# Kernel tuning notes

Measured on AMD Instinct MI355X. Metric: run time of the kernel, lower is better.

## Reference

```python
import math
import jax, jax.numpy as jnp
import numpy as np

WS = [2048, 4096, 8192]
RS = [1, 2, 4]
HEAD_IDX = 0


def build_indices(n):
    """Static dilated gather indices: concat of every segment's strided slice.

    Matches _prepare_sparse_indices for the chosen (ws, rs, n), which yields
    zero padding (each segment contributes exactly max_subatt_n indices).
    """
    max_m = min(n, max(w // r for w, r in zip(WS, RS)))
    parts = []
    for w, r in zip(WS, RS):
        offset = HEAD_IDX % r
        for s in range(0, n, w):
            seg = np.arange(s, min(s + w, n))[offset::r]
            assert len(seg) == max_m, "config chosen to avoid padding"
            parts.append(seg)
    return np.concatenate(parts).astype(np.int32), max_m


def _forward(x, Wq, Wk, Wv):
    b, n, c = x.shape
    idx_np, m = build_indices(n)
    idx = jnp.asarray(idx_np)            # [S], S = num_subatt * m
    S = idx_np.shape[0]
    nb = S // m                          # number of sub-attention windows

    # gather -> [b, S, c] -> batched windows [b*nb, m, c]
    bx = x[:, idx, :].reshape(b * nb, m, c)

    # single-head causal attention on each window, also return softmax denoms
    scale = 1.0 / math.sqrt(c)
    q = bx @ Wq
    k = bx @ Wk
    v = bx @ Wv
    logits = jnp.einsum('bqc,bkc->bqk', q, k) * scale
    causal = jnp.tril(jnp.ones((m, m), dtype=bool))
    logits = jnp.where(causal, logits, -jnp.inf)
    lse = jax.scipy.special.logsumexp(logits, axis=-1)   # [b*nb, m]
    probs = jnp.exp(logits - lse[..., None])
    o = jnp.einsum('bqk,bkc->bqc', probs, v)             # [b*nb, m, c]
    denoms = jnp.exp(lse)                                 # softmax denominators

    o = o.reshape(b, S, c)
    denoms = denoms.reshape(b, S)

    # _mix_outputs: scatter-add denoms per target position, reweight, scatter-add outputs
    denom_sums = jnp.zeros((b, n), x.dtype).at[:, idx].add(denoms)
    alphas = denoms / denom_sums[:, idx]                  # [b, S]
    out = jnp.zeros((b, n, c), x.dtype).at[:, idx, :].add(o * alphas[..., None])
    return out


def setup_inputs() -> dict:
    key = jax.random.key(0)
    kx, kq, kk, kv = jax.random.split(key, 4)
    b, n, c = 4, 8192, 64
    s = 1.0 / math.sqrt(c)
    return {
        'x': jax.random.normal(kx, (b, n, c), dtype=jnp.float32),
        'Wq': jax.random.normal(kq, (c, c), dtype=jnp.float32) * s,
        'Wk': jax.random.normal(kk, (c, c), dtype=jnp.float32) * s,
        'Wv': jax.random.normal(kv, (c, c), dtype=jnp.float32) * s,
    }


def reference(x, Wq, Wk, Wv):
    return _forward(x, Wq, Wk, Wv)
```

## Files before the change

### kernel.cpp

```cpp
#include <hip/hip_runtime.h>
#include <math.h>

#define NB   4
#define NSEQ 8192
#define CDIM 64
#define M    2048
#define NW   7
#define NBLK2 40

typedef _Float16 half8 __attribute__((ext_vector_type(8)));
typedef __fp16 fp16x2 __attribute__((ext_vector_type(2)));
typedef float f32x4 __attribute__((ext_vector_type(4)));
typedef unsigned short u16x4 __attribute__((ext_vector_type(4)));

#if defined(__has_builtin) && __has_builtin(__builtin_amdgcn_exp2f)
#define EXP2(x) __builtin_amdgcn_exp2f(x)
#else
#define EXP2(x) __expf((x) * 0.69314718056f)
#endif

#define QSCALE 0.1803368801111204f
#define PBIAS 4.0f

#define K_OFF   0
#define VT_OFF  8192
#define VT_STRIDE 80
#define VT_BUF  5120

__device__ __forceinline__ int win_base(int w) {
    return (w < 4) ? (w << 11) : ((w < 6) ? ((w - 4) << 12) : 0);
}
__device__ __forceinline__ int win_stride(int w) {
    return (w < 4) ? 1 : ((w < 6) ? 2 : 4);
}

__global__ __launch_bounds__(256, 1) void qkv_proj(
        const float* __restrict__ x,
        const float* __restrict__ Wq, const float* __restrict__ Wk,
        const float* __restrict__ Wv,
        _Float16* __restrict__ Qg, _Float16* __restrict__ Kg,
        _Float16* __restrict__ Vg) {
    const int t = threadIdx.x;
    const int wid = t >> 6, lane = t & 63, l15 = lane & 15, quad = lane >> 4;

    half8 wb[3][2][4];
#pragma unroll
    for (int m = 0; m < 3; ++m) {
        const float* Wm = (m == 0) ? Wq : ((m == 1) ? Wk : Wv);
        const float sc = (m == 0) ? QSCALE : 1.0f;
#pragma unroll
        for (int kh = 0; kh < 2; ++kh)
#pragma unroll
            for (int nt = 0; nt < 4; ++nt) {
                float f[8];
#pragma unroll
                for (int j = 0; j < 8; ++j)
                    f[j] = Wm[(kh * 32 + quad * 8 + j) * 64 + nt * 16 + l15] * sc;
                union { fp16x2 h[4]; half8 v; } u;
#pragma unroll
                for (int p = 0; p < 4; ++p)
                    u.h[p] = __builtin_amdgcn_cvt_pkrtz(f[2 * p], f[2 * p + 1]);
                wb[m][kh][nt] = u.v;
            }
    }

    const int rowbase = blockIdx.x * 128 + wid * 32;
#pragma unroll
    for (int mt = 0; mt < 2; ++mt) {
        const int r0 = rowbase + mt * 16;
        half8 xa[2];
#pragma unroll
        for (int kh = 0; kh < 2; ++kh) {
            const float* xr = x + (size_t)(r0 + l15) * 64 + kh * 32 + quad * 8;
            const float4 a = *(const float4*)xr;
            const float4 b2 = *(const float4*)(xr + 4);
            union { fp16x2 h[4]; half8 v; } u;
            u.h[0] = __builtin_amdgcn_cvt_pkrtz(a.x, a.y);
            u.h[1] = __builtin_amdgcn_cvt_pkrtz(a.z, a.w);
            u.h[2] = __builtin_amdgcn_cvt_pkrtz(b2.x, b2.y);
            u.h[3] = __builtin_amdgcn_cvt_pkrtz(b2.z, b2.w);
            xa[kh] = u.v;
        }
#pragma unroll
        for (int m = 0; m < 3; ++m) {
            f32x4 acc[4];
#pragma unroll
            for (int nt = 0; nt < 4; ++nt) {
                acc[nt] = (f32x4){0.f, 0.f, 0.f, 0.f};
                acc[nt] = __builtin_amdgcn_mfma_f32_16x16x32_f16(xa[0], wb[m][0][nt], acc[nt], 0, 0, 0);
                acc[nt] = __builtin_amdgcn_mfma_f32_16x16x32_f16(xa[1], wb[m][1][nt], acc[nt], 0, 0, 0);
            }
            _Float16* outp = (m == 0) ? Qg : ((m == 1) ? Kg : Vg);
#pragma unroll
            for (int nt = 0; nt < 4; ++nt)
#pragma unroll
                for (int j = 0; j < 4; ++j)
                    outp[(size_t)(r0 + quad * 4 + j) * 64 + nt * 16 + l15] =
                        (_Float16)acc[nt][j];
        }
    }
}

__global__ __launch_bounds__(256, 4) void attn(
        const _Float16* __restrict__ Qg, const _Float16* __restrict__ Kg,
        const _Float16* __restrict__ Vg,
        _Float16* __restrict__ Op, float* __restrict__ LSEp) {
    __shared__ __align__(16) char smem[18432];

    int id = 39 - (int)blockIdx.x;
    int QT, ci;
    if (id < 4)       { QT = id;              ci = 0; }
    else if (id < 12) { int r = id - 4;  QT = 4  + (r >> 1); ci = r & 1; }
    else if (id < 24) { int r = id - 12; int q3 = r / 3; QT = 8 + q3; ci = r - 3 * q3; }
    else              { int r = id - 24; QT = 12 + (r >> 2); ci = r & 3; }
    const int w = blockIdx.y, b = blockIdx.z;
    const int base = win_base(w), stride = win_stride(w);
    const int g = QT >> 2;
    const int cb = 2 * g * (g + 1) + (QT & 3) * (g + 1);
    const int outblk = (b * NW + w) * NBLK2 + cb + ci;
    const int kt0 = ci * 16;
    const int ktmax = 4 * QT + 4;
    const int kt1 = (kt0 + 16 < ktmax) ? kt0 + 16 : ktmax;

    const _Float16* Qb = Qg + (size_t)b * NSEQ * 64;
    const _Float16* Kb = Kg + (size_t)b * NSEQ * 64;
    const _Float16* Vb = Vg + (size_t)b * NSEQ * 64;

    const int t = threadIdx.x;
    const int wid = t >> 6, lane = t & 63, l15 = lane & 15, quad = lane >> 4;

    const int sr = t >> 3, sch = t & 7;
    const int c4 = t & 15, kq = t >> 4;
    const int vd0 = 4 * c4;

    const size_t qr0 = (size_t)(base + stride * (QT * 128 + 16 * wid + l15)) * 64;
    const size_t qr1 = (size_t)(base + stride * (QT * 128 + 64 + 16 * wid + l15)) * 64;
    const half8 qa00 = *(const half8*)(Qb + qr0 + quad * 8);
    const half8 qa01 = *(const half8*)(Qb + qr0 + 32 + quad * 8);
    const half8 qa10 = *(const half8*)(Qb + qr1 + quad * 8);
    const half8 qa11 = *(const half8*)(Qb + qr1 + 32 + quad * 8);

    f32x4 oacc0[4], oacc1[4];
    float l0 = 0.f, l1 = 0.f;
#pragma unroll
    for (int ns = 0; ns < 4; ++ns) {
        oacc0[ns] = (f32x4){0.f, 0.f, 0.f, 0.f};
        oacc1[ns] = (f32x4){0.f, 0.f, 0.f, 0.f};
    }

    half8 pk;
    u16x4 pv0, pv1;

    {
        const size_t ka = (size_t)(base + stride * (kt0 * 32 + sr)) * 64 + sch * 8;
        pk = *(const half8*)(Kb + ka);
        const size_t va = (size_t)(base + stride * (kt0 * 32 + kq)) * 64 + vd0;
        pv0 = *(const u16x4*)(Vb + va);
        pv1 = *(const u16x4*)(Vb + va + (size_t)stride * 16 * 64);
        char* Kd = smem + K_OFF;
        char* Vd = smem + VT_OFF;
        *(half8*)(Kd + sr * 128 + ((sch ^ (sr & 7)) * 16)) = pk;
#pragma unroll
        for (int i = 0; i < 4; ++i) {
            int d = vd0 + i;
            unsigned int pkw = (unsigned int)pv0[i] | ((unsigned int)pv1[i] << 16);
            int ch = ((kq >> 2) ^ (d >> 4) ^ (d & 3) ^ ((d >> 2) & 3)) & 3;
            *(unsigned int*)(Vd + d * VT_STRIDE + ch * 16 + (kq & 3) * 4) = pkw;
        }
    }

    int cur = 0;
    for (int kt = kt0; kt < kt1; ++kt) {
        __syncthreads();
        const bool pf = (kt + 1 < kt1);
        if (pf) {
            const size_t ka = (size_t)(base + stride * ((kt + 1) * 32 + sr)) * 64 + sch * 8;
            pk = *(const half8*)(Kb + ka);
            const size_t va = (size_t)(base + stride * ((kt + 1) * 32 + kq)) * 64 + vd0;
            pv0 = *(const u16x4*)(Vb + va);
            pv1 = *(const u16x4*)(Vb + va + (size_t)stride * 16 * 64);
        }

        const char* Kd = smem + K_OFF + cur * 4096;
        const char* Vd = smem + VT_OFF + cur * VT_BUF;

        half8 kb[2][2];
#pragma unroll
        for (int ns = 0; ns < 2; ++ns) {
            const int krow = ns * 16 + l15, swk = krow & 7;
            kb[ns][0] = *(const half8*)(Kd + krow * 128 + ((quad ^ swk) * 16));
            kb[ns][1] = *(const half8*)(Kd + krow * 128 + (((quad + 4) ^ swk) * 16));
        }
        f32x4 sa0[2], sa1[2];
        __builtin_amdgcn_s_setprio(1);
#pragma unroll
        for (int ns = 0; ns < 2; ++ns) {
            f32x4 c0 = (f32x4){0.f, 0.f, 0.f, 0.f};
            c0 = __builtin_amdgcn_mfma_f32_16x16x32_f16(kb[ns][0], qa00, c0, 0, 0, 0);
            c0 = __builtin_amdgcn_mfma_f32_16x16x32_f16(kb[ns][1], qa01, c0, 0, 0, 0);
            sa0[ns] = c0;
            f32x4 c1 = (f32x4){0.f, 0.f, 0.f, 0.f};
            c1 = __builtin_amdgcn_mfma_f32_16x16x32_f16(kb[ns][0], qa10, c1, 0, 0, 0);
            c1 = __builtin_amdgcn_mfma_f32_16x16x32_f16(kb[ns][1], qa11, c1, 0, 0, 0);
            sa1[ns] = c1;
        }
        __builtin_amdgcn_s_setprio(0);
        if (kt >= 4 * QT) {
            const int q0 = QT * 128 + 16 * wid + l15 - kt * 32;
            const int kvb = quad * 4;
#pragma unroll
            for (int ns = 0; ns < 2; ++ns)
#pragma unroll
                for (int j = 0; j < 4; ++j) {
                    if (kvb + ns * 16 + j > q0)      sa0[ns][j] = -1e30f;
                    if (kvb + ns * 16 + j > q0 + 64) sa1[ns][j] = -1e30f;
                }
        }

        half8 vb[4];
#pragma unroll
        for (int ns = 0; ns < 4; ++ns) {
            const int d = ns * 16 + l15;
            const int ch = (quad ^ (d >> 4) ^ (d & 3) ^ ((d >> 2) & 3)) & 3;
            vb[ns] = *(const half8*)(Vd + d * VT_STRIDE + ch * 16);
        }

        {
            union { fp16x2 h[4]; half8 v; } pu;
#pragma unroll
            for (int u = 0; u < 4; ++u) {
                float pA = EXP2(sa0[0][u] - PBIAS);
                float pB = EXP2(sa0[1][u] - PBIAS);
                l0 += pA + pB;
                pu.h[u] = __builtin_amdgcn_cvt_pkrtz(pA, pB);
            }
            __builtin_amdgcn_s_setprio(1);
#pragma unroll
            for (int ns = 0; ns < 4; ++ns)
                oacc0[ns] = __builtin_amdgcn_mfma_f32_16x16x32_f16(pu.v, vb[ns], oacc0[ns], 0, 0, 0);
            __builtin_amdgcn_s_setprio(0);
        }
        {
            union { fp16x2 h[4]; half8 v; } pu;
#pragma unroll
            for (int u = 0; u < 4; ++u) {
                float pA = EXP2(sa1[0][u] - PBIAS);
                float pB = EXP2(sa1[1][u] - PBIAS);
                l1 += pA + pB;
                pu.h[u] = __builtin_amdgcn_cvt_pkrtz(pA, pB);
            }
            __builtin_amdgcn_s_setprio(1);
#pragma unroll
            for (int ns = 0; ns < 4; ++ns)
                oacc1[ns] = __builtin_amdgcn_mfma_f32_16x16x32_f16(pu.v, vb[ns], oacc1[ns], 0, 0, 0);
            __builtin_amdgcn_s_setprio(0);
        }

        if (pf) {
            char* Kn = smem + K_OFF + (cur ^ 1) * 4096;
            char* Vn = smem + VT_OFF + (cur ^ 1) * VT_BUF;
            *(half8*)(Kn + sr * 128 + ((sch ^ (sr & 7)) * 16)) = pk;
#pragma unroll
            for (int i = 0; i < 4; ++i) {
                int d = vd0 + i;
                unsigned int pkw = (unsigned int)pv0[i] | ((unsigned int)pv1[i] << 16);
                int ch = ((kq >> 2) ^ (d >> 4) ^ (d & 3) ^ ((d >> 2) & 3)) & 3;
                *(unsigned int*)(Vn + d * VT_STRIDE + ch * 16 + (kq & 3) * 4) = pkw;
            }
        }
        cur ^= 1;
    }

    l0 += __shfl_xor(l0, 16, 64);
    l0 += __shfl_xor(l0, 32, 64);
    l1 += __shfl_xor(l1, 16, 64);
    l1 += __shfl_xor(l1, 32, 64);
    if (quad == 0) {
        LSEp[(size_t)outblk * 128 + 16 * wid + l15]      = __logf(l0);
        LSEp[(size_t)outblk * 128 + 64 + 16 * wid + l15] = __logf(l1);
    }
    const int qrow0 = 16 * wid + quad * 4;
#pragma unroll
    for (int j = 0; j < 4; ++j) {
        const float inv0 = 1.0f / __shfl(l0, quad * 4 + j, 64);
        const float inv1 = 1.0f / __shfl(l1, quad * 4 + j, 64);
        const size_t r0off = ((size_t)outblk * 128 + qrow0 + j) * 64 + l15;
        const size_t r1off = ((size_t)outblk * 128 + 64 + qrow0 + j) * 64 + l15;
#pragma unroll
        for (int ns = 0; ns < 4; ++ns) {
            Op[r0off + ns * 16] = (_Float16)(oacc0[ns][j] * inv0);
            Op[r1off + ns * 16] = (_Float16)(oacc1[ns][j] * inv1);
        }
    }
}

typedef _Float16 half8v __attribute__((ext_vector_type(8)));
__global__ __launch_bounds__(256) void mix_out(
        const _Float16* __restrict__ Op, const float* __restrict__ LSEp,
        float* __restrict__ out) {
    int gid = blockIdx.x * 256 + threadIdx.x;
    int f8 = gid & 7;
    int tpos = (gid >> 3) & (NSEQ - 1);
    int b = gid >> 16;

    int idx[12];
    float lse[12];

    {
        int w = tpos >> 11, j = tpos & (M - 1);
        int QT = j >> 7, gg = QT >> 2, q = j & 127;
        int cbase = 2 * gg * (gg + 1) + (QT & 3) * (gg + 1);
        int bb = ((b * NW + w) * NBLK2 + cbase) * 128 + q;
        int cmax = j >> 9;
#pragma unroll
        for (int c = 0; c < 4; ++c) {
            int cc = (c <= cmax) ? c : cmax;
            idx[c] = bb + cc * 128;
            float v = LSEp[idx[c]];
            lse[c] = (c <= cmax) ? v : -1e30f;
        }
    }
    {
        int act = ((tpos & 1) == 0);
        int w = 4 + (tpos >> 12), j = (tpos & 4095) >> 1;
        int QT = j >> 7, gg = QT >> 2, q = j & 127;
        int cbase = 2 * gg * (gg + 1) + (QT & 3) * (gg + 1);
        int bb = ((b * NW + w) * NBLK2 + cbase) * 128 + q;
        int cmax = j >> 9;
#pragma unroll
        for (int c = 0; c < 4; ++c) {
            int cc = (c <= cmax) ? c : cmax;
            idx[4 + c] = bb + cc * 128;
            float v = LSEp[idx[4 + c]];
            lse[4 + c] = (act && c <= cmax) ? v : -1e30f;
        }
    }
    {
        int act = ((tpos & 3) == 0);
        int j = tpos >> 2;
        int QT = j >> 7, gg = QT >> 2, q = j & 127;
        int cbase = 2 * gg * (gg + 1) + (QT & 3) * (gg + 1);
        int bb = ((b * NW + 6) * NBLK2 + cbase) * 128 + q;
        int cmax = j >> 9;
#pragma unroll
        for (int c = 0; c < 4; ++c) {
            int cc = (c <= cmax) ? c : cmax;
            idx[8 + c] = bb + cc * 128;
            float v = LSEp[idx[8 + c]];
            lse[8 + c] = (act && c <= cmax) ? v : -1e30f;
        }
    }

    half8v v[12];
#pragma unroll
    for (int i = 0; i < 12; ++i)
        v[i] = *(const half8v*)(Op + (size_t)idx[i] * 64 + f8 * 8);

    float Mx = -1e30f;
#pragma unroll
    for (int i = 0; i < 12; ++i) Mx = fmaxf(Mx, lse[i]);

    float acc[8];
#pragma unroll
    for (int k = 0; k < 8; ++k) acc[k] = 0.f;
    float wsum = 0.f;
#pragma unroll
    for (int i = 0; i < 12; ++i) {
        float a = __expf(lse[i] - Mx);
        wsum += a;
#pragma unroll
        for (int k = 0; k < 8; ++k) acc[k] += a * (float)v[i][k];
    }
    float inv = 1.0f / wsum;
    size_t o = ((size_t)b * NSEQ + tpos) * 64 + f8 * 8;
    float4 r0 = make_float4(acc[0] * inv, acc[1] * inv, acc[2] * inv, acc[3] * inv);
    float4 r1 = make_float4(acc[4] * inv, acc[5] * inv, acc[6] * inv, acc[7] * inv);
    *(float4*)&out[o] = r0;
    *(float4*)&out[o + 4] = r1;
}

extern "C" void kernel_launch(void* const* d_in, const int* in_sizes, int n_in,
                              void* d_out, int out_size, void* d_ws, size_t ws_size,
                              hipStream_t stream) {
    const float* x  = (const float*)d_in[0];
    const float* Wq = (const float*)d_in[1];
    const float* Wk = (const float*)d_in[2];
    const float* Wv = (const float*)d_in[3];
    float* out = (float*)d_out;

    const size_t QN = (size_t)NB * NSEQ * CDIM;
    _Float16* Qg = (_Float16*)d_ws;
    _Float16* Kg = Qg + QN;
    _Float16* Vg = Kg + QN;
    _Float16* Op = Vg + QN;
    float* LSEp  = (float*)(Op + (size_t)NB * NW * NBLK2 * 128 * 64);

    qkv_proj<<<NB * NSEQ / 128, 256, 0, stream>>>(x, Wq, Wk, Wv, Qg, Kg, Vg);
    attn<<<dim3(NBLK2, NW, NB), 256, 0, stream>>>(Qg, Kg, Vg, Op, LSEp);
    mix_out<<<(NB * NSEQ * 8) / 256, 256, 0, stream>>>(Op, LSEp, out);
}
```

Before: 113.2 us.

## Halve split-K chunk size in attention and merge partials with raw sums

Each attention work item now covers 8 key tiles instead of 16, so every window and batch gets 72 blocks instead of 40, with a new triangular index mapping. The aim is better load balance and occupancy across the GPU's compute units. The attention kernel now stores raw softmax row sums instead of log-sum-exp values. The merge kernel therefore skips the max-subtraction and exp pass, weights the partials directly, and exits early for inactive dilated windows. In exchange, the partial-output workspace roughly doubles and the merge kernel may read up to 24 partials per position instead of 12. Dropping the max-subtraction relies on the kernel's fixed softmax bias to keep the raw sums in range.

```diff
diff --git a/kernel.cpp b/kernel.cpp
--- a/kernel.cpp
+++ b/kernel.cpp
@@ -6,7 +6,7 @@
 #define CDIM 64
 #define M    2048
 #define NW   7
-#define NBLK2 40
+#define NBLK2 72
 
 typedef _Float16 half8 __attribute__((ext_vector_type(8)));
 typedef __fp16 fp16x2 __attribute__((ext_vector_type(2)));
@@ -104,23 +104,24 @@
 __global__ __launch_bounds__(256, 4) void attn(
         const _Float16* __restrict__ Qg, const _Float16* __restrict__ Kg,
         const _Float16* __restrict__ Vg,
-        _Float16* __restrict__ Op, float* __restrict__ LSEp) {
+        _Float16* __restrict__ Op, float* __restrict__ Lp) {
     __shared__ __align__(16) char smem[18432];
 
-    int id = 39 - (int)blockIdx.x;
-    int QT, ci;
-    if (id < 4)       { QT = id;              ci = 0; }
-    else if (id < 12) { int r = id - 4;  QT = 4  + (r >> 1); ci = r & 1; }
-    else if (id < 24) { int r = id - 12; int q3 = r / 3; QT = 8 + q3; ci = r - 3 * q3; }
-    else              { int r = id - 24; QT = 12 + (r >> 2); ci = r & 3; }
+    const int idx = (NBLK2 - 1) - (int)blockIdx.x;
+    int QT = 0;
+    QT += (idx >= 1);  QT += (idx >= 2);  QT += (idx >= 4);  QT += (idx >= 6);
+    QT += (idx >= 9);  QT += (idx >= 12); QT += (idx >= 16); QT += (idx >= 20);
+    QT += (idx >= 25); QT += (idx >= 30); QT += (idx >= 36); QT += (idx >= 42);
+    QT += (idx >= 49); QT += (idx >= 56); QT += (idx >= 64);
+    const int k2 = QT >> 1;
+    const int cb = (QT & 1) ? (k2 + 1) * (k2 + 1) : k2 * (k2 + 1);
+    const int ci = idx - cb;
     const int w = blockIdx.y, b = blockIdx.z;
     const int base = win_base(w), stride = win_stride(w);
-    const int g = QT >> 2;
-    const int cb = 2 * g * (g + 1) + (QT & 3) * (g + 1);
     const int outblk = (b * NW + w) * NBLK2 + cb + ci;
-    const int kt0 = ci * 16;
+    const int kt0 = ci * 8;
     const int ktmax = 4 * QT + 4;
-    const int kt1 = (kt0 + 16 < ktmax) ? kt0 + 16 : ktmax;
+    const int kt1 = (kt0 + 8 < ktmax) ? kt0 + 8 : ktmax;
 
     const _Float16* Qb = Qg + (size_t)b * NSEQ * 64;
     const _Float16* Kb = Kg + (size_t)b * NSEQ * 64;
@@ -276,8 +277,8 @@
     l1 += __shfl_xor(l1, 16, 64);
     l1 += __shfl_xor(l1, 32, 64);
     if (quad == 0) {
-        LSEp[(size_t)outblk * 128 + 16 * wid + l15]      = __logf(l0);
-        LSEp[(size_t)outblk * 128 + 64 + 16 * wid + l15] = __logf(l1);
+        Lp[(size_t)outblk * 128 + 16 * wid + l15]      = l0;
+        Lp[(size_t)outblk * 128 + 64 + 16 * wid + l15] = l1;
     }
     const int qrow0 = 16 * wid + quad * 4;
 #pragma unroll
@@ -296,81 +297,73 @@
 
 typedef _Float16 half8v __attribute__((ext_vector_type(8)));
 __global__ __launch_bounds__(256) void mix_out(
-        const _Float16* __restrict__ Op, const float* __restrict__ LSEp,
+        const _Float16* __restrict__ Op, const float* __restrict__ Lp,
         float* __restrict__ out) {
     int gid = blockIdx.x * 256 + threadIdx.x;
     int f8 = gid & 7;
     int tpos = (gid >> 3) & (NSEQ - 1);
     int b = gid >> 16;
 
-    int idx[12];
-    float lse[12];
+    float wsum = 0.f;
+    float acc[8];
+#pragma unroll
+    for (int k = 0; k < 8; ++k) acc[k] = 0.f;
 
     {
         int w = tpos >> 11, j = tpos & (M - 1);
-        int QT = j >> 7, gg = QT >> 2, q = j & 127;
-        int cbase = 2 * gg * (gg + 1) + (QT & 3) * (gg + 1);
+        int QT = j >> 7, q = j & 127, k2 = QT >> 1;
+        int cbase = (QT & 1) ? (k2 + 1) * (k2 + 1) : k2 * (k2 + 1);
         int bb = ((b * NW + w) * NBLK2 + cbase) * 128 + q;
-        int cmax = j >> 9;
-#pragma unroll
-        for (int c = 0; c < 4; ++c) {
+        int cmax = j >> 8;
+#pragma unroll
+        for (int c = 0; c < 8; ++c) {
             int cc = (c <= cmax) ? c : cmax;
-            idx[c] = bb + cc * 128;
-            float v = LSEp[idx[c]];
-            lse[c] = (c <= cmax) ? v : -1e30f;
-        }
-    }
-    {
-        int act = ((tpos & 1) == 0);
+            int ix = bb + cc * 128;
+            float li = Lp[ix];
+            li = (c <= cmax) ? li : 0.f;
+            half8v v = *(const half8v*)(Op + (size_t)ix * 64 + f8 * 8);
+            wsum += li;
+#pragma unroll
+            for (int k = 0; k < 8; ++k) acc[k] += li * (float)v[k];
+        }
+    }
+    if (!(tpos & 1)) {
         int w = 4 + (tpos >> 12), j = (tpos & 4095) >> 1;
-        int QT = j >> 7, gg = QT >> 2, q = j & 127;
-        int cbase = 2 * gg * (gg + 1) + (QT & 3) * (gg + 1);
+        int QT = j >> 7, q = j & 127, k2 = QT >> 1;
+        int cbase = (QT & 1) ? (k2 + 1) * (k2 + 1) : k2 * (k2 + 1);
         int bb = ((b * NW + w) * NBLK2 + cbase) * 128 + q;
-        int cmax = j >> 9;
-#pragma unroll
-        for (int c = 0; c < 4; ++c) {
+        int cmax = j >> 8;
+#pragma unroll
+        for (int c = 0; c < 8; ++c) {
             int cc = (c <= cmax) ? c : cmax;
-            idx[4 + c] = bb + cc * 128;
-            float v = LSEp[idx[4 + c]];
-            lse[4 + c] = (act && c <= cmax) ? v : -1e30f;
-        }
-    }
-    {
-        int act = ((tpos & 3) == 0);
+            int ix = bb + cc * 128;
+            float li = Lp[ix];
+            li = (c <= cmax) ? li : 0.f;
+            half8v v = *(const half8v*)(Op + (size_t)ix * 64 + f8 * 8);
+            wsum += li;
+#pragma unroll
+            for (int k = 0; k < 8; ++k) acc[k] += li * (float)v[k];
+        }
+    }
+    if (!(tpos & 3)) {
         int j = tpos >> 2;
-        int QT = j >> 7, gg = QT >> 2, q = j & 127;
-        int cbase = 2 * gg * (gg + 1) + (QT & 3) * (gg + 1);
+        int QT = j >> 7, q = j & 127, k2 = QT >> 1;
+        int cbase = (QT & 1) ? (k2 + 1) * (k2 + 1) : k2 * (k2 + 1);
         int bb = ((b * NW + 6) * NBLK2 + cbase) * 128 + q;
-        int cmax = j >> 9;
-#pragma unroll
-        for (int c = 0; c < 4; ++c) {
+        int cmax = j >> 8;
+#pragma unroll
+        for (int c = 0; c < 8; ++c) {
             int cc = (c <= cmax) ? c : cmax;
-            idx[8 + c] = bb + cc * 128;
-            float v = LSEp[idx[8 + c]];
-            lse[8 + c] = (act && c <= cmax) ? v : -1e30f;
-        }
-    }
-
-    half8v v[12];
-#pragma unroll
-    for (int i = 0; i < 12; ++i)
-        v[i] = *(const half8v*)(Op + (size_t)idx[i] * 64 + f8 * 8);
-
-    float Mx = -1e30f;
-#pragma unroll
-    for (int i = 0; i < 12; ++i) Mx = fmaxf(Mx, lse[i]);
-
-    float acc[8];
-#pragma unroll
-    for (int k = 0; k < 8; ++k) acc[k] = 0.f;
-    float wsum = 0.f;
-#pragma unroll
-    for (int i = 0; i < 12; ++i) {
-        float a = __expf(lse[i] - Mx);
-        wsum += a;
-#pragma unroll
-        for (int k = 0; k < 8; ++k) acc[k] += a * (float)v[i][k];
-    }
+            int ix = bb + cc * 128;
+            float li = Lp[ix];
+            li = (c <= cmax) ? li : 0.f;
+            half8v v = *(const half8v*)(Op + (size_t)ix * 64 + f8 * 8);
+            wsum += li;
+#pragma unroll
+            for (int k = 0; k < 8; ++k) acc[k] += li * (float)v[k];
+        }
+    }
+
     float inv = 1.0f / wsum;
     size_t o = ((size_t)b * NSEQ + tpos) * 64 + f8 * 8;
     float4 r0 = make_float4(acc[0] * inv, acc[1] * inv, acc[2] * inv, acc[3] * inv);
@@ -393,9 +386,9 @@
     _Float16* Kg = Qg + QN;
     _Float16* Vg = Kg + QN;
     _Float16* Op = Vg + QN;
-    float* LSEp  = (float*)(Op + (size_t)NB * NW * NBLK2 * 128 * 64);
+    float* Lp   = (float*)(Op + (size_t)NB * NW * NBLK2 * 128 * 64);
 
     qkv_proj<<<NB * NSEQ / 128, 256, 0, stream>>>(x, Wq, Wk, Wv, Qg, Kg, Vg);
-    attn<<<dim3(NBLK2, NW, NB), 256, 0, stream>>>(Qg, Kg, Vg, Op, LSEp);
-    mix_out<<<(NB * NSEQ * 8) / 256, 256, 0, stream>>>(Op, LSEp, out);
-}
+    attn<<<dim3(NBLK2, NW, NB), 256, 0, stream>>>(Qg, Kg, Vg, Op, Lp);
+    mix_out<<<(NB * NSEQ * 8) / 256, 256, 0, stream>>>(Op, Lp, out);
+}
```

After: 110.7 us, median of 3. 2.1% less time.
